# Performance work log

Hardware: AMD Instinct MI355X
Metric: run time of the kernel (lower is better)

The kernel has to match this reference:

```python
import jax, jax.numpy as jnp
import numpy as np

# ---- ATSSPostProcessor config ----
PRE_NMS_THRESH = 0.05
PRE_NMS_TOP_N  = 400      # k candidates per image (pre_nms_top_n)
NMS_THRESH     = 0.4
POST_TOP_N     = 100      # fpn_post_nms_top_n
MIN_SIZE       = 0.0
NUM_ANGLE_BINS = 90
BBOX_W         = (10.0, 10.0, 5.0, 5.0)   # box_coder xywh weights; angle is passthrough (argmax-90 deg)
N, C, H, W     = 4, 15, 256, 256           # A=1 anchor per location
STRIDE, ANCHOR_SIZE = 8.0, 64.0
MAXV = 16                                   # vertex buffer for quad-quad clipping


def setup_inputs():
    key = jax.random.key(0)
    k1, k2, k3, k4 = jax.random.split(key, 4)
    box_cls = jax.random.normal(k1, (N, C, H, W), jnp.float32) - 2.0  # sigmoid ~0.12 avg -> plenty of candidates
    box_regression = jax.random.normal(k2, (N, 4, H, W), jnp.float32) * 0.5
    centerness = jax.random.normal(k3, (N, 1, H, W), jnp.float32)
    angle = jax.random.normal(k4, (N, NUM_ANGLE_BINS, H, W), jnp.float32)
    # xywha anchors on the stride-8 grid, row-major (H, W) to match permute_and_flatten ordering
    ys, xs = jnp.meshgrid(jnp.arange(H, dtype=jnp.float32), jnp.arange(W, dtype=jnp.float32), indexing='ij')
    cx = (xs.reshape(-1) + 0.5) * STRIDE
    cy = (ys.reshape(-1) + 0.5) * STRIDE
    wh = jnp.full((H * W,), ANCHOR_SIZE, jnp.float32)
    a0 = jnp.zeros((H * W,), jnp.float32)
    anchors = jnp.broadcast_to(jnp.stack([cx, cy, wh, wh, a0], -1), (N, H * W, 5))
    return {"box_cls": box_cls, "box_regression": box_regression, "centerness": centerness,
            "angle": angle, "anchors": jnp.asarray(anchors)}


def xywha_to_corners(b):
    # b [..., 5] (cx,cy,w,h,angle_deg) -> [..., 4, 2], CCW order
    cx, cy, w, h, a = b[..., 0], b[..., 1], b[..., 2], b[..., 3], b[..., 4]
    t = a * (jnp.pi / 180.0)
    c, s = jnp.cos(t), jnp.sin(t)
    ox = jnp.asarray([1., -1., -1., 1.], b.dtype) * (w[..., None] * 0.5)
    oy = jnp.asarray([1., 1., -1., -1.], b.dtype) * (h[..., None] * 0.5)
    x = cx[..., None] + ox * c[..., None] - oy * s[..., None]
    y = cy[..., None] + ox * s[..., None] + oy * c[..., None]
    return jnp.stack([x, y], -1)


def _clip_edge(poly, n, p1, p2):
    # Sutherland-Hodgman: clip CCW polygon (poly[:n]) against half-plane left of p1->p2
    e = p2 - p1
    d = e[0] * (poly[:, 1] - p1[1]) - e[1] * (poly[:, 0] - p1[0])  # >= 0 is inside
    def body(i, carry):
        out, m = carry
        j = jnp.where(i == n - 1, 0, i + 1)
        cur, nxt, dc, dn = poly[i], poly[j], d[i], d[j]
        denom = dc - dn
        denom = jnp.where(jnp.abs(denom) < 1e-8, 1e-8, denom)
        ip = cur + (dc / denom) * (nxt - cur)
        act = i < n
        a1 = act & (dc >= 0)
        out = out.at[m].set(jnp.where(a1, cur, out[m]))
        m = m + a1.astype(jnp.int32)
        a2 = act & ((dc >= 0) != (dn >= 0))
        out = out.at[m].set(jnp.where(a2, ip, out[m]))
        m = m + a2.astype(jnp.int32)
        return out, m
    return jax.lax.fori_loop(0, 8, body, (jnp.zeros_like(poly), jnp.int32(0)))


def _quad_inter_area(c1, c2):
    # intersection area of two CCW quads via polygon clipping + shoelace
    poly = jnp.zeros((MAXV, 2), c1.dtype).at[:4].set(c1)
    n = jnp.int32(4)
    def edge(e, carry):
        poly, n = carry
        return _clip_edge(poly, n, c2[e], c2[(e + 1) % 4])
    poly, n = jax.lax.fori_loop(0, 4, edge, (poly, n))
    idx = jnp.arange(MAXV)
    j = jnp.where(idx == n - 1, 0, idx + 1)
    mask = idx < n
    terms = poly[:, 0] * poly[j, 1] - poly[j, 0] * poly[:, 1]
    return 0.5 * jnp.abs(jnp.sum(jnp.where(mask, terms, 0.0)))


def _riou_matrix(boxes):                        # [k,5] -> [k,k] rotated IoU
    corners = xywha_to_corners(boxes)           # [k,4,2]
    areas = boxes[:, 2] * boxes[:, 3]
    def one(ci, ai):
        def two(cj, aj):
            inter = _quad_inter_area(ci, cj)
            return inter / (ai + aj - inter + 1e-7)
        return jax.vmap(two)(corners, areas)
    return jax.vmap(one)(corners, areas)


@jax.jit
def _forward(box_cls, box_regression, centerness, angle, anchors):
    n, c, h, w = box_cls.shape
    K, k = h * w, PRE_NMS_TOP_N
    # permute_and_flatten + activations
    cls = jax.nn.sigmoid(box_cls).transpose(0, 2, 3, 1).reshape(n, K, c)
    reg = box_regression.transpose(0, 2, 3, 1).reshape(n, K, 4)
    ctr = jax.nn.sigmoid(centerness).reshape(n, K)
    ang = jax.nn.softmax(angle.transpose(0, 2, 3, 1).reshape(n, K, NUM_ANGLE_BINS), axis=-1)
    # pre-nms threshold on raw sigmoid cls, topk on cls*centerness
    cand = cls > PRE_NMS_THRESH
    comb = cls * ctr[:, :, None]
    flat = jnp.where(cand, comb, -1.0).reshape(n, K * c)
    topv, topi = jax.lax.top_k(flat, k)          # sorted descending
    valid = topv > 0.0                           # emulates per_pre_nms_top_n clamp
    loc = topi // c
    labels = topi % c + 1
    reg_s = jnp.take_along_axis(reg, loc[..., None], axis=1)       # [n,k,4]
    anc_s = jnp.take_along_axis(anchors, loc[..., None], axis=1)   # [n,k,5]
    ang_s = jnp.take_along_axis(ang, loc[..., None], axis=1)       # [n,k,90]
    pred_angle = jnp.argmax(ang_s, axis=-1).astype(reg_s.dtype) - 90.0
    # box_coder.decode (xywh deltas, angle passthrough)
    wx, wy, ww, wh = BBOX_W
    dx, dy = reg_s[..., 0] / wx, reg_s[..., 1] / wy
    dw = jnp.clip(reg_s[..., 2] / ww, -10.0, 4.0)
    dh = jnp.clip(reg_s[..., 3] / wh, -10.0, 4.0)
    acx, acy, aw, ah = anc_s[..., 0], anc_s[..., 1], anc_s[..., 2], anc_s[..., 3]
    boxes = jnp.stack([dx * aw + acx, dy * ah + acy,
                       aw * jnp.exp(dw), ah * jnp.exp(dh), pred_angle], -1)
    valid = valid & (boxes[..., 2] >= MIN_SIZE) & (boxes[..., 3] >= MIN_SIZE)
    scores = jnp.where(valid, jnp.sqrt(jnp.maximum(topv, 0.0)), 0.0)
    # class-aware rotated NMS (boxlist_ml_rnms): IoU only within same class
    iou = jax.lax.stop_gradient(jax.vmap(_riou_matrix)(boxes))     # [n,k,k]
    same = labels[:, :, None] == labels[:, None, :]
    iou = jnp.where(same, iou, 0.0)
    idxs = jnp.arange(k)
    def body(i, keep):
        sup = keep[:, i][:, None] & (iou[:, i, :] > NMS_THRESH) & (idxs[None, :] > i)
        return keep & ~sup
    keep = jax.lax.fori_loop(0, k, body, valid)
    # keep top fpn_post_nms_top_n by score
    fscore = jnp.where(keep, scores, -1.0)
    fv, fi = jax.lax.top_k(fscore, POST_TOP_N)
    fvalid = fv > 0.0
    fboxes = jnp.take_along_axis(boxes, fi[..., None], axis=1)
    flabels = jnp.take_along_axis(labels, fi, axis=1)
    corners = xywha_to_corners(fboxes).reshape(n, POST_TOP_N, 8)   # convert('xyxyxyxy')
    out = jnp.concatenate([corners,
                           jnp.maximum(fv, 0.0)[..., None],
                           flabels.astype(corners.dtype)[..., None],
                           fvalid.astype(corners.dtype)[..., None]], -1)
    return out * fvalid[..., None].astype(out.dtype)   # [N, POST_TOP_N, 11]


def reference(box_cls, box_regression, centerness, angle, anchors):
    return _forward(box_cls, box_regression, centerness, angle, anchors)
```

## Files before the change

### kernel.cpp

```cpp
#include <hip/hip_runtime.h>
#include <math.h>

#define NIMG 4
#define NCLS 15
#define HW 65536
#define NANG 90
#define KTOP 400
#define POSTN 100
#define NBINS 4096
#define CAP 4096

#define HIST_OFF   0
#define CNT_OFF    65536
#define SUPT_OFF   65600
#define ZERO_BYTES 165952
#define CAND_OFF   165952
#define SKEY_OFF   297024
#define COR_OFF    309824
#define AREA_OFF   361024
#define LAB_OFF    367424
#define SC_OFF     373824
#define VAL_OFF    380224
#define CCX_OFF    386624
#define CCY_OFF    393024
#define CRAD_OFF   399424

__device__ __forceinline__ float sigmoidf(float x) {
    return 1.0f / (1.0f + expf(-x));
}

__global__ __launch_bounds__(256)
void k_hist(const float* __restrict__ cls, const float* __restrict__ ctr,
            int* __restrict__ hist) {
    __shared__ int sh[NBINS];
    const int n = blockIdx.y;
    const int p2 = (blockIdx.x * 256 + threadIdx.x) * 2;
    for (int b = threadIdx.x; b < NBINS; b += 256) sh[b] = 0;
    __syncthreads();
    float2 cv2 = *(const float2*)(ctr + n * HW + p2);
    float cv[2] = {sigmoidf(cv2.x), sigmoidf(cv2.y)};
    for (int j = 0; j < NCLS; ++j) {
        float2 s2 = *(const float2*)(cls + (size_t)(n * NCLS + j) * HW + p2);
        float sv[2] = {s2.x, s2.y};
#pragma unroll
        for (int e = 0; e < 2; ++e) {
            float s = sigmoidf(sv[e]);
            if (s > 0.05f) {
                float comb = s * cv[e];
                int b = (int)(comb * 4096.0f);
                b = b < 0 ? 0 : (b > NBINS - 1 ? NBINS - 1 : b);
                atomicAdd(&sh[b], 1);
            }
        }
    }
    __syncthreads();
    for (int b = threadIdx.x; b < NBINS; b += 256) {
        int v = sh[b];
        if (v) atomicAdd(&hist[n * NBINS + b], v);
    }
}

__global__ __launch_bounds__(256)
void k_collect(const float* __restrict__ cls, const float* __restrict__ ctr,
               const int* __restrict__ hist, int* __restrict__ cnt,
               unsigned long long* __restrict__ cand) {
    const int n = blockIdx.y;
    __shared__ int part[256];
    __shared__ int s_t;
    {
        const int* hb = hist + n * NBINS;
        int s = 0;
        int base = threadIdx.x * 16;
        for (int b = 0; b < 16; ++b) s += hb[base + b];
        part[threadIdx.x] = s;
        if (threadIdx.x == 0) s_t = 0;
        __syncthreads();
        for (int off = 1; off < 256; off <<= 1) {
            int v = part[threadIdx.x] +
                    ((threadIdx.x + off < 256) ? part[threadIdx.x + off] : 0);
            __syncthreads();
            part[threadIdx.x] = v;
            __syncthreads();
        }
        int sg = threadIdx.x;
        int suf = part[sg];
        int above = (sg == 255) ? 0 : part[sg + 1];
        if (suf >= KTOP && above < KTOP) {
            int a2 = above, t = sg * 16;
            for (int b = sg * 16 + 15; b >= sg * 16; --b) {
                a2 += hb[b];
                if (a2 >= KTOP) { t = b; break; }
            }
            s_t = t;
        }
        __syncthreads();
    }
    const int t = s_t;
    const int p2 = (blockIdx.x * 256 + threadIdx.x) * 2;
    float2 cv2 = *(const float2*)(ctr + n * HW + p2);
    float cv[2] = {sigmoidf(cv2.x), sigmoidf(cv2.y)};
    for (int j = 0; j < NCLS; ++j) {
        float2 s2 = *(const float2*)(cls + (size_t)(n * NCLS + j) * HW + p2);
        float sv[2] = {s2.x, s2.y};
#pragma unroll
        for (int e = 0; e < 2; ++e) {
            float s = sigmoidf(sv[e]);
            if (s > 0.05f) {
                float comb = s * cv[e];
                int b = (int)(comb * 4096.0f);
                b = b < 0 ? 0 : (b > NBINS - 1 ? NBINS - 1 : b);
                if (b >= t) {
                    int pos = atomicAdd(&cnt[n], 1);
                    if (pos < CAP) {
                        unsigned int fb  = __float_as_uint(comb);
                        unsigned int idx = (unsigned int)((p2 + e) * NCLS + j);
                        cand[n * CAP + pos] =
                            ((unsigned long long)fb << 32) | (unsigned long long)(~idx);
                    }
                }
            }
        }
    }
}

__global__ __launch_bounds__(256)
void k_select(const unsigned long long* __restrict__ cand, const int* __restrict__ cnt,
              unsigned long long* __restrict__ skey) {
    const int n = blockIdx.x;
    __shared__ unsigned long long key[CAP];
    int c = cnt[n];
    if (c > CAP) c = CAP;
    int S = 512;
    while (S < c) S <<= 1;
    for (int t = threadIdx.x; t < S; t += 256)
        key[t] = (t < c) ? cand[n * CAP + t] : 0ULL;
    __syncthreads();
    for (int k = 2; k <= S; k <<= 1) {
        for (int j = k >> 1; j > 0; j >>= 1) {
            for (int i = threadIdx.x; i < S; i += 256) {
                int l = i ^ j;
                if (l > i) {
                    unsigned long long a = key[i], b = key[l];
                    bool up = ((i & k) == 0);
                    if ((a > b) == up) { key[i] = b; key[l] = a; }
                }
            }
            __syncthreads();
        }
    }
    for (int r = threadIdx.x; r < KTOP; r += 256)
        skey[n * KTOP + r] = key[S - 1 - r];
}

__global__ __launch_bounds__(64)
void k_decode(const unsigned long long* __restrict__ skey,
              const float* __restrict__ reg, const float* __restrict__ ang,
              const float* __restrict__ anchors,
              float* __restrict__ cor, float* __restrict__ area, int* __restrict__ lab,
              float* __restrict__ sc, int* __restrict__ val,
              float* __restrict__ ccx, float* __restrict__ ccy, float* __restrict__ crad) {
#pragma clang fp contract(off)
    const int r = blockIdx.x;
    const int n = blockIdx.y;
    const int l = threadIdx.x;
    const int base = n * KTOP + r;
    unsigned long long kk = skey[base];
    if (kk == 0ULL) {
        if (l == 0) {
            val[base] = 0; sc[base] = 0.0f; lab[base] = 0; area[base] = 0.0f;
            ccx[base] = 0.0f; ccy[base] = 0.0f; crad[base] = 0.0f;
            for (int q = 0; q < 8; ++q) cor[base * 8 + q] = 0.0f;
        }
        return;
    }
    unsigned int idx = ~((unsigned int)kk);
    int loc = (int)(idx / 15u);
    const float* ap = ang + ((size_t)n * NANG) * HW + loc;
    float bv = -INFINITY; int bb = 1000;
    for (int b = l; b < NANG; b += 64) {
        float v = ap[(size_t)b * HW];
        if (v > bv) { bv = v; bb = b; }
    }
    for (int off = 32; off > 0; off >>= 1) {
        float ov = __shfl_down(bv, off);
        int   ob = __shfl_down(bb, off);
        if (ov > bv || (ov == bv && ob < bb)) { bv = ov; bb = ob; }
    }
    if (l == 0) {
        int cl = (int)(idx % 15u);
        float topv = __uint_as_float((unsigned int)(kk >> 32));
        const float* rp = reg + ((size_t)n * 4) * HW + loc;
        float dx = rp[0] / 10.0f;
        float dy = rp[HW] / 10.0f;
        float dw = rp[2 * (size_t)HW] / 5.0f;
        float dh = rp[3 * (size_t)HW] / 5.0f;
        dw = fminf(fmaxf(dw, -10.0f), 4.0f);
        dh = fminf(fmaxf(dh, -10.0f), 4.0f);
        const float* an = anchors + ((size_t)n * HW + loc) * 5;
        float acx = an[0], acy = an[1], aw = an[2], ah = an[3];
        float bcx = dx * aw + acx;
        float bcy = dy * ah + acy;
        float bw = aw * expf(dw);
        float bh = ah * expf(dh);
        float pa = (float)bb - 90.0f;
        float th = pa * (float)0.017453292519943295;
        float cth = cosf(th), sth = sinf(th);
        float hw2 = bw * 0.5f, hh2 = bh * 0.5f;
        const float oxs[4] = {1.0f, -1.0f, -1.0f, 1.0f};
        const float oys[4] = {1.0f, 1.0f, -1.0f, -1.0f};
        for (int q = 0; q < 4; ++q) {
            float ox = oxs[q] * hw2, oy = oys[q] * hh2;
            cor[base * 8 + 2 * q]     = bcx + ox * cth - oy * sth;
            cor[base * 8 + 2 * q + 1] = bcy + ox * sth + oy * cth;
        }
        val[base] = 1;
        sc[base] = sqrtf(topv);
        lab[base] = cl + 1;
        area[base] = bw * bh;
        ccx[base] = bcx; ccy[base] = bcy;
        crad[base] = 0.5f * sqrtf(bw * bw + bh * bh);
    }
}

__device__ __forceinline__ float arr_get8(const float* a, int idx) {
    float r = a[0];
#pragma unroll
    for (int s = 1; s < 8; ++s) r = (s == idx) ? a[s] : r;
    return r;
}
__device__ __forceinline__ void arr_set8(float* a, int idx, float v) {
#pragma unroll
    for (int s = 0; s < 8; ++s) a[s] = (s == idx) ? v : a[s];
}

__device__ float quad_inter_area(const float* c1x, const float* c1y,
                                 const float* c2x, const float* c2y) {
#pragma clang fp contract(off)
    float px[8], py[8], qx[8], qy[8];
    int n = 4;
#pragma unroll
    for (int i = 0; i < 8; ++i) { px[i] = (i < 4) ? c1x[i] : 0.0f;
                                  py[i] = (i < 4) ? c1y[i] : 0.0f;
                                  qx[i] = 0.0f; qy[i] = 0.0f; }
#pragma unroll
    for (int e = 0; e < 4; ++e) {
        float p1x = c2x[e], p1y = c2y[e];
        int e2 = (e + 1) & 3;
        float ex = c2x[e2] - p1x, ey = c2y[e2] - p1y;
        int m = 0;
#pragma unroll
        for (int i = 0; i < 8; ++i) {
            if (i < n) {
                int j = (i == n - 1) ? 0 : i + 1;
                float cxi = px[i], cyi = py[i];
                float cxj = arr_get8(px, j), cyj = arr_get8(py, j);
                float dc = ex * (cyi - p1y) - ey * (cxi - p1x);
                float dn = ex * (cyj - p1y) - ey * (cxj - p1x);
                bool ic = (dc >= 0.0f), in2 = (dn >= 0.0f);
                if (ic) { arr_set8(qx, m, cxi); arr_set8(qy, m, cyi); ++m; }
                if (ic != in2) {
                    float denom = dc - dn;
                    if (fabsf(denom) < 1e-8f) denom = 1e-8f;
                    float tp = dc / denom;
                    arr_set8(qx, m, cxi + tp * (cxj - cxi));
                    arr_set8(qy, m, cyi + tp * (cyj - cyi));
                    ++m;
                }
            }
        }
        n = m;
        if (n == 0) return 0.0f;
#pragma unroll
        for (int i = 0; i < 8; ++i) { px[i] = qx[i]; py[i] = qy[i]; }
    }
    float ssum = 0.0f;
#pragma unroll
    for (int i = 0; i < 8; ++i) {
        if (i < n) {
            int j = (i == n - 1) ? 0 : i + 1;
            ssum += px[i] * arr_get8(py, j) - arr_get8(px, j) * py[i];
        }
    }
    return 0.5f * fabsf(ssum);
}

__global__ __launch_bounds__(256)
void k_pairs(const float* __restrict__ cor, const float* __restrict__ area,
             const int* __restrict__ lab,
             const float* __restrict__ ccx, const float* __restrict__ ccy,
             const float* __restrict__ crad,
             unsigned long long* __restrict__ supT) {
#pragma clang fp contract(off)
    const int n = blockIdx.y;
    const int p = blockIdx.x * 256 + threadIdx.x;
    if (p >= KTOP * KTOP) return;
    const int i = p / KTOP;
    const int j = p - i * KTOP;
    if (j <= i) return;
    const int base = n * KTOP;
    const int li = lab[base + i];
    if (li == 0 || lab[base + j] != li) return;
    float dx = ccx[base + i] - ccx[base + j];
    float dy = ccy[base + i] - ccy[base + j];
    float rr = crad[base + i] + crad[base + j];
    if (dx * dx + dy * dy > rr * rr) return;
    float cix[4], ciy[4], cjx[4], cjy[4];
    for (int q = 0; q < 4; ++q) {
        cix[q] = cor[(base + i) * 8 + 2 * q]; ciy[q] = cor[(base + i) * 8 + 2 * q + 1];
        cjx[q] = cor[(base + j) * 8 + 2 * q]; cjy[q] = cor[(base + j) * 8 + 2 * q + 1];
    }
    float inter = quad_inter_area(cix, ciy, cjx, cjy);
    float iou = inter / (area[base + i] + area[base + j] - inter + 1e-7f);
    if (iou > 0.4f) {
        atomicOr(&supT[((size_t)(n * 7 + (j >> 6)) * 7 + (i >> 6)) * 64 + (j & 63)],
                 1ULL << (i & 63));
    }
}

__global__ __launch_bounds__(64)
void k_nms_out(const unsigned long long* __restrict__ supT,
               const int* __restrict__ val,
               const float* __restrict__ cor, const float* __restrict__ sc,
               const int* __restrict__ lab, float* __restrict__ out) {
    const int n = blockIdx.x;
    const int l = threadIdx.x;
    unsigned removed = 0;
#pragma unroll
    for (int t = 0; t < 7; ++t) {
        int r = 64 * t + l;
        int v = (r < KTOP) ? val[n * KTOP + r] : 0;
        if (!v) removed |= (1u << t);
    }
    unsigned long long cm[7][7];
#pragma unroll
    for (int t = 0; t < 7; ++t)
#pragma unroll
        for (int rb = 0; rb < 7; ++rb)
            cm[t][rb] = supT[((size_t)(n * 7 + t) * 7 + rb) * 64 + l];
#pragma unroll
    for (int rb = 0; rb < 7; ++rb) {
        const int lim = (rb == 6) ? (KTOP - 384) : 64;
        for (int ib = 0; ib < lim; ++ib) {
            unsigned rm = (unsigned)__builtin_amdgcn_readlane((int)removed, ib);
            if (!((rm >> rb) & 1u)) {
                removed |= ((unsigned)((cm[0][rb] >> ib) & 1ULL));
                removed |= ((unsigned)((cm[1][rb] >> ib) & 1ULL)) << 1;
                removed |= ((unsigned)((cm[2][rb] >> ib) & 1ULL)) << 2;
                removed |= ((unsigned)((cm[3][rb] >> ib) & 1ULL)) << 3;
                removed |= ((unsigned)((cm[4][rb] >> ib) & 1ULL)) << 4;
                removed |= ((unsigned)((cm[5][rb] >> ib) & 1ULL)) << 5;
                removed |= ((unsigned)((cm[6][rb] >> ib) & 1ULL)) << 6;
            }
        }
    }
    __shared__ int order[POSTN];
    int rank = 0;
#pragma unroll
    for (int t = 0; t < 7; ++t) {
        bool kb = !((removed >> t) & 1u) && (64 * t + l < KTOP);
        unsigned long long m = __ballot(kb);
        int my = rank + __popcll(m & ((1ULL << l) - 1ULL));
        if (kb && my < POSTN) order[my] = 64 * t + l;
        rank += __popcll(m);
    }
    int kcnt = rank < POSTN ? rank : POSTN;
    __syncthreads();
    for (int e = l; e < POSTN * 11; e += 64) {
        int r = e / 11, c = e - r * 11;
        float v = 0.0f;
        if (r < kcnt) {
            int i = order[r];
            int b = n * KTOP + i;
            if (c < 8)       v = cor[b * 8 + c];
            else if (c == 8) v = sc[b];
            else if (c == 9) v = (float)lab[b];
            else             v = 1.0f;
        }
        out[(n * POSTN + r) * 11 + c] = v;
    }
}

extern "C" void kernel_launch(void* const* d_in, const int* in_sizes, int n_in,
                              void* d_out, int out_size, void* d_ws, size_t ws_size,
                              hipStream_t stream) {
    const float* box_cls = (const float*)d_in[0];
    const float* box_reg = (const float*)d_in[1];
    const float* ctr     = (const float*)d_in[2];
    const float* ang     = (const float*)d_in[3];
    const float* anchors = (const float*)d_in[4];
    float* out = (float*)d_out;
    char* ws = (char*)d_ws;

    int* hist = (int*)(ws + HIST_OFF);
    int* cnt  = (int*)(ws + CNT_OFF);
    unsigned long long* supT = (unsigned long long*)(ws + SUPT_OFF);
    unsigned long long* cand = (unsigned long long*)(ws + CAND_OFF);
    unsigned long long* skey = (unsigned long long*)(ws + SKEY_OFF);
    float* cor  = (float*)(ws + COR_OFF);
    float* area = (float*)(ws + AREA_OFF);
    int* lab    = (int*)(ws + LAB_OFF);
    float* sc   = (float*)(ws + SC_OFF);
    int* val    = (int*)(ws + VAL_OFF);
    float* ccx  = (float*)(ws + CCX_OFF);
    float* ccy  = (float*)(ws + CCY_OFF);
    float* crad = (float*)(ws + CRAD_OFF);

    hipMemsetAsync(d_ws, 0, ZERO_BYTES, stream);
    k_hist   <<<dim3(HW / 512, NIMG), 256, 0, stream>>>(box_cls, ctr, hist);
    k_collect<<<dim3(HW / 512, NIMG), 256, 0, stream>>>(box_cls, ctr, hist, cnt, cand);
    k_select <<<NIMG, 256, 0, stream>>>(cand, cnt, skey);
    k_decode <<<dim3(KTOP, NIMG), 64, 0, stream>>>(skey, box_reg, ang, anchors,
                                                   cor, area, lab, sc, val, ccx, ccy, crad);
    k_pairs  <<<dim3((KTOP * KTOP + 255) / 256, NIMG), 256, 0, stream>>>(
                 cor, area, lab, ccx, ccy, crad, supT);
    k_nms_out<<<NIMG, 64, 0, stream>>>(supT, val, cor, sc, lab, out);
}
```

Baseline: 248.8 us.

## Fuse histogram and collect into cooperative kernel; merge sort with decode

Replaces the memset, histogram and collect kernels with one cooperative kernel. It zeroes the workspace in-kernel, keeps the per-pixel combined scores in registers, and uses two grid-wide syncs instead of separate launches. The bitonic sort and box decode are merged into one kernel, so sorted keys go straight from shared memory to decode without a global skey buffer. The cost is that decode now runs on only 4 blocks with serial 90-bin angle argmax per thread instead of 1600 wave-parallel blocks, and the cooperative launch requires all 512 blocks to be co-resident. Blocks also add their partial histograms to hist after only one grid sync following the zeroing, which is correct but tightly ordered.

```diff
diff --git a/kernel.cpp b/kernel.cpp
--- a/kernel.cpp
+++ b/kernel.cpp
@@ -1,5 +1,8 @@
 #include <hip/hip_runtime.h>
+#include <hip/hip_cooperative_groups.h>
 #include <math.h>
+
+namespace cg = cooperative_groups;
 
 #define NIMG 4
 #define NCLS 15
@@ -15,7 +18,6 @@
 #define SUPT_OFF   65600
 #define ZERO_BYTES 165952
 #define CAND_OFF   165952
-#define SKEY_OFF   297024
 #define COR_OFF    309824
 #define AREA_OFF   361024
 #define LAB_OFF    367424
@@ -30,43 +32,56 @@
 }
 
 __global__ __launch_bounds__(256)
-void k_hist(const float* __restrict__ cls, const float* __restrict__ ctr,
-            int* __restrict__ hist) {
-    __shared__ int sh[NBINS];
+void k_fused_select(const float* __restrict__ cls, const float* __restrict__ ctr,
+                    int* wsz, int* hist, int* cnt,
+                    unsigned long long* __restrict__ cand) {
+    __shared__ int sh[2][NBINS];
+    __shared__ int part[256];
+    __shared__ int s_t;
     const int n = blockIdx.y;
     const int p2 = (blockIdx.x * 256 + threadIdx.x) * 2;
-    for (int b = threadIdx.x; b < NBINS; b += 256) sh[b] = 0;
+
+    {
+        const int gtid = (blockIdx.y * gridDim.x + blockIdx.x) * 256 + threadIdx.x;
+        for (int z = gtid; z < (ZERO_BYTES / 4); z += 131072) wsz[z] = 0;
+    }
+    for (int b = threadIdx.x; b < NBINS; b += 256) { sh[0][b] = 0; sh[1][b] = 0; }
+
+    float cb[15][2];
+    {
+        float2 cv2 = *(const float2*)(ctr + n * HW + p2);
+        float cv0 = sigmoidf(cv2.x), cv1 = sigmoidf(cv2.y);
+#pragma unroll
+        for (int j = 0; j < NCLS; ++j) {
+            float2 s2 = *(const float2*)(cls + (size_t)(n * NCLS + j) * HW + p2);
+            float s0 = sigmoidf(s2.x), s1 = sigmoidf(s2.y);
+            cb[j][0] = (s0 > 0.05f) ? s0 * cv0 : -1.0f;
+            cb[j][1] = (s1 > 0.05f) ? s1 * cv1 : -1.0f;
+        }
+    }
     __syncthreads();
-    float2 cv2 = *(const float2*)(ctr + n * HW + p2);
-    float cv[2] = {sigmoidf(cv2.x), sigmoidf(cv2.y)};
+    const int subh = threadIdx.x & 1;
+#pragma unroll
     for (int j = 0; j < NCLS; ++j) {
-        float2 s2 = *(const float2*)(cls + (size_t)(n * NCLS + j) * HW + p2);
-        float sv[2] = {s2.x, s2.y};
 #pragma unroll
         for (int e = 0; e < 2; ++e) {
-            float s = sigmoidf(sv[e]);
-            if (s > 0.05f) {
-                float comb = s * cv[e];
-                int b = (int)(comb * 4096.0f);
+            float c = cb[j][e];
+            if (c >= 0.0f) {
+                int b = (int)(c * 4096.0f);
                 b = b < 0 ? 0 : (b > NBINS - 1 ? NBINS - 1 : b);
-                atomicAdd(&sh[b], 1);
+                atomicAdd(&sh[subh][b], 1);
             }
         }
     }
     __syncthreads();
+    cg::this_grid().sync();
+
     for (int b = threadIdx.x; b < NBINS; b += 256) {
-        int v = sh[b];
+        int v = sh[0][b] + sh[1][b];
         if (v) atomicAdd(&hist[n * NBINS + b], v);
     }
-}
-
-__global__ __launch_bounds__(256)
-void k_collect(const float* __restrict__ cls, const float* __restrict__ ctr,
-               const int* __restrict__ hist, int* __restrict__ cnt,
-               unsigned long long* __restrict__ cand) {
-    const int n = blockIdx.y;
-    __shared__ int part[256];
-    __shared__ int s_t;
+    cg::this_grid().sync();
+
     {
         const int* hb = hist + n * NBINS;
         int s = 0;
@@ -96,23 +111,18 @@
         __syncthreads();
     }
     const int t = s_t;
-    const int p2 = (blockIdx.x * 256 + threadIdx.x) * 2;
-    float2 cv2 = *(const float2*)(ctr + n * HW + p2);
-    float cv[2] = {sigmoidf(cv2.x), sigmoidf(cv2.y)};
+#pragma unroll
     for (int j = 0; j < NCLS; ++j) {
-        float2 s2 = *(const float2*)(cls + (size_t)(n * NCLS + j) * HW + p2);
-        float sv[2] = {s2.x, s2.y};
 #pragma unroll
         for (int e = 0; e < 2; ++e) {
-            float s = sigmoidf(sv[e]);
-            if (s > 0.05f) {
-                float comb = s * cv[e];
-                int b = (int)(comb * 4096.0f);
+            float c = cb[j][e];
+            if (c >= 0.0f) {
+                int b = (int)(c * 4096.0f);
                 b = b < 0 ? 0 : (b > NBINS - 1 ? NBINS - 1 : b);
                 if (b >= t) {
                     int pos = atomicAdd(&cnt[n], 1);
                     if (pos < CAP) {
-                        unsigned int fb  = __float_as_uint(comb);
+                        unsigned int fb  = __float_as_uint(c);
                         unsigned int idx = (unsigned int)((p2 + e) * NCLS + j);
                         cand[n * CAP + pos] =
                             ((unsigned long long)fb << 32) | (unsigned long long)(~idx);
@@ -124,8 +134,13 @@
 }
 
 __global__ __launch_bounds__(256)
-void k_select(const unsigned long long* __restrict__ cand, const int* __restrict__ cnt,
-              unsigned long long* __restrict__ skey) {
+void k_sortdecode(const unsigned long long* __restrict__ cand, const int* __restrict__ cnt,
+                  const float* __restrict__ reg, const float* __restrict__ ang,
+                  const float* __restrict__ anchors,
+                  float* __restrict__ cor, float* __restrict__ area, int* __restrict__ lab,
+                  float* __restrict__ sc, int* __restrict__ val,
+                  float* __restrict__ ccx, float* __restrict__ ccy, float* __restrict__ crad) {
+#pragma clang fp contract(off)
     const int n = blockIdx.x;
     __shared__ unsigned long long key[CAP];
     int c = cnt[n];
@@ -148,45 +163,24 @@
             __syncthreads();
         }
     }
-    for (int r = threadIdx.x; r < KTOP; r += 256)
-        skey[n * KTOP + r] = key[S - 1 - r];
-}
-
-__global__ __launch_bounds__(64)
-void k_decode(const unsigned long long* __restrict__ skey,
-              const float* __restrict__ reg, const float* __restrict__ ang,
-              const float* __restrict__ anchors,
-              float* __restrict__ cor, float* __restrict__ area, int* __restrict__ lab,
-              float* __restrict__ sc, int* __restrict__ val,
-              float* __restrict__ ccx, float* __restrict__ ccy, float* __restrict__ crad) {
-#pragma clang fp contract(off)
-    const int r = blockIdx.x;
-    const int n = blockIdx.y;
-    const int l = threadIdx.x;
-    const int base = n * KTOP + r;
-    unsigned long long kk = skey[base];
-    if (kk == 0ULL) {
-        if (l == 0) {
+    for (int r = threadIdx.x; r < KTOP; r += 256) {
+        const int base = n * KTOP + r;
+        unsigned long long kk = key[S - 1 - r];
+        if (kk == 0ULL) {
             val[base] = 0; sc[base] = 0.0f; lab[base] = 0; area[base] = 0.0f;
             ccx[base] = 0.0f; ccy[base] = 0.0f; crad[base] = 0.0f;
             for (int q = 0; q < 8; ++q) cor[base * 8 + q] = 0.0f;
-        }
-        return;
-    }
-    unsigned int idx = ~((unsigned int)kk);
-    int loc = (int)(idx / 15u);
-    const float* ap = ang + ((size_t)n * NANG) * HW + loc;
-    float bv = -INFINITY; int bb = 1000;
-    for (int b = l; b < NANG; b += 64) {
-        float v = ap[(size_t)b * HW];
-        if (v > bv) { bv = v; bb = b; }
-    }
-    for (int off = 32; off > 0; off >>= 1) {
-        float ov = __shfl_down(bv, off);
-        int   ob = __shfl_down(bb, off);
-        if (ov > bv || (ov == bv && ob < bb)) { bv = ov; bb = ob; }
-    }
-    if (l == 0) {
+            continue;
+        }
+        unsigned int idx = ~((unsigned int)kk);
+        int loc = (int)(idx / 15u);
+        const float* ap = ang + ((size_t)n * NANG) * HW + loc;
+        float bv = -INFINITY; int bb = 0;
+#pragma unroll
+        for (int b = 0; b < NANG; ++b) {
+            float v = ap[(size_t)b * HW];
+            if (v > bv) { bv = v; bb = b; }
+        }
         int cl = (int)(idx % 15u);
         float topv = __uint_as_float((unsigned int)(kk >> 32));
         const float* rp = reg + ((size_t)n * 4) * HW + loc;
@@ -208,6 +202,7 @@
         float hw2 = bw * 0.5f, hh2 = bh * 0.5f;
         const float oxs[4] = {1.0f, -1.0f, -1.0f, 1.0f};
         const float oys[4] = {1.0f, 1.0f, -1.0f, -1.0f};
+#pragma unroll
         for (int q = 0; q < 4; ++q) {
             float ox = oxs[q] * hw2, oy = oys[q] * hh2;
             cor[base * 8 + 2 * q]     = bcx + ox * cth - oy * sth;
@@ -391,11 +386,11 @@
     float* out = (float*)d_out;
     char* ws = (char*)d_ws;
 
+    int* wsz  = (int*)(ws + HIST_OFF);
     int* hist = (int*)(ws + HIST_OFF);
     int* cnt  = (int*)(ws + CNT_OFF);
     unsigned long long* supT = (unsigned long long*)(ws + SUPT_OFF);
     unsigned long long* cand = (unsigned long long*)(ws + CAND_OFF);
-    unsigned long long* skey = (unsigned long long*)(ws + SKEY_OFF);
     float* cor  = (float*)(ws + COR_OFF);
     float* area = (float*)(ws + AREA_OFF);
     int* lab    = (int*)(ws + LAB_OFF);
@@ -405,13 +400,15 @@
     float* ccy  = (float*)(ws + CCY_OFF);
     float* crad = (float*)(ws + CRAD_OFF);
 
-    hipMemsetAsync(d_ws, 0, ZERO_BYTES, stream);
-    k_hist   <<<dim3(HW / 512, NIMG), 256, 0, stream>>>(box_cls, ctr, hist);
-    k_collect<<<dim3(HW / 512, NIMG), 256, 0, stream>>>(box_cls, ctr, hist, cnt, cand);
-    k_select <<<NIMG, 256, 0, stream>>>(cand, cnt, skey);
-    k_decode <<<dim3(KTOP, NIMG), 64, 0, stream>>>(skey, box_reg, ang, anchors,
-                                                   cor, area, lab, sc, val, ccx, ccy, crad);
-    k_pairs  <<<dim3((KTOP * KTOP + 255) / 256, NIMG), 256, 0, stream>>>(
-                 cor, area, lab, ccx, ccy, crad, supT);
+    {
+        void* args[] = {(void*)&box_cls, (void*)&ctr, (void*)&wsz,
+                        (void*)&hist, (void*)&cnt, (void*)&cand};
+        hipLaunchCooperativeKernel((const void*)k_fused_select,
+                                   dim3(HW / 512, NIMG), dim3(256), args, 0, stream);
+    }
+    k_sortdecode<<<NIMG, 256, 0, stream>>>(cand, cnt, box_reg, ang, anchors,
+                                           cor, area, lab, sc, val, ccx, ccy, crad);
+    k_pairs<<<dim3((KTOP * KTOP + 255) / 256, NIMG), 256, 0, stream>>>(
+             cor, area, lab, ccx, ccy, crad, supT);
     k_nms_out<<<NIMG, 64, 0, stream>>>(supT, val, cor, sc, lab, out);
 }
```

After: 470.3 us. 89.0% more time.

## Stage high-score candidates during histogram pass and merge collect into select

Applied to the files above, without the earlier changes.

The histogram kernel now also writes candidates above a fixed score-bin floor into a per-image staging buffer. This removes the second full pass over the class and centerness tensors that the collect kernel used to make. A new combined select kernel filters the staged entries by the top-k threshold and sorts them in shared memory. It falls back to a single-block full rescan when the staging overflows or the threshold falls below the floor. The supT zeroing also moves from the memset into the decode kernel to shrink the memset, and one kernel launch is removed. The fixed floor bin is tuned to the expected score distribution, so if it is wrong the slow single-block fallback runs.

```diff
diff --git a/kernel.cpp b/kernel.cpp
--- a/kernel.cpp
+++ b/kernel.cpp
@@ -9,21 +9,25 @@
 #define POSTN 100
 #define NBINS 4096
 #define CAP 4096
+#define SCAP 49152
+#define SBUF 512
+#define FLOOR_BIN 1434
 
 #define HIST_OFF   0
-#define CNT_OFF    65536
+#define SCNT_OFF   65536
+#define SFLAG_OFF  65552
+#define ZERO_BYTES 65600
 #define SUPT_OFF   65600
-#define ZERO_BYTES 165952
-#define CAND_OFF   165952
-#define SKEY_OFF   297024
-#define COR_OFF    309824
-#define AREA_OFF   361024
-#define LAB_OFF    367424
-#define SC_OFF     373824
-#define VAL_OFF    380224
-#define CCX_OFF    386624
-#define CCY_OFF    393024
-#define CRAD_OFF   399424
+#define STAGE_OFF  165952
+#define SKEY_OFF   1738816
+#define COR_OFF    1751616
+#define AREA_OFF   1802816
+#define LAB_OFF    1809216
+#define SC_OFF     1815616
+#define VAL_OFF    1822016
+#define CCX_OFF    1828416
+#define CCY_OFF    1834816
+#define CRAD_OFF   1841216
 
 __device__ __forceinline__ float sigmoidf(float x) {
     return 1.0f / (1.0f + expf(-x));
@@ -31,11 +35,15 @@
 
 __global__ __launch_bounds__(256)
 void k_hist(const float* __restrict__ cls, const float* __restrict__ ctr,
-            int* __restrict__ hist) {
+            int* __restrict__ hist, int* __restrict__ scnt,
+            unsigned long long* __restrict__ stage, int* __restrict__ sflag) {
     __shared__ int sh[NBINS];
+    __shared__ unsigned long long sbuf[SBUF];
+    __shared__ int scount, sbase;
     const int n = blockIdx.y;
     const int p2 = (blockIdx.x * 256 + threadIdx.x) * 2;
     for (int b = threadIdx.x; b < NBINS; b += 256) sh[b] = 0;
+    if (threadIdx.x == 0) scount = 0;
     __syncthreads();
     float2 cv2 = *(const float2*)(ctr + n * HW + p2);
     float cv[2] = {sigmoidf(cv2.x), sigmoidf(cv2.y)};
@@ -50,6 +58,15 @@
                 int b = (int)(comb * 4096.0f);
                 b = b < 0 ? 0 : (b > NBINS - 1 ? NBINS - 1 : b);
                 atomicAdd(&sh[b], 1);
+                if (b >= FLOOR_BIN) {
+                    int m = atomicAdd(&scount, 1);
+                    if (m < SBUF) {
+                        unsigned int fb  = __float_as_uint(comb);
+                        unsigned int idx = (unsigned int)((p2 + e) * NCLS + j);
+                        sbuf[m] = ((unsigned long long)fb << 32) |
+                                  (unsigned long long)(~idx);
+                    }
+                }
             }
         }
     }
@@ -58,22 +75,36 @@
         int v = sh[b];
         if (v) atomicAdd(&hist[n * NBINS + b], v);
     }
+    if (threadIdx.x == 0) {
+        int c = scount;
+        if (c > SBUF) { atomicOr(sflag, 1); c = SBUF; }
+        sbase = atomicAdd(&scnt[n], c);
+    }
+    __syncthreads();
+    int c = scount < SBUF ? scount : SBUF;
+    int base = sbase;
+    for (int m = threadIdx.x; m < c; m += 256) {
+        int g = base + m;
+        if (g < SCAP) stage[n * SCAP + g] = sbuf[m];
+    }
 }
 
 __global__ __launch_bounds__(256)
-void k_collect(const float* __restrict__ cls, const float* __restrict__ ctr,
-               const int* __restrict__ hist, int* __restrict__ cnt,
-               unsigned long long* __restrict__ cand) {
-    const int n = blockIdx.y;
+void k_selstage(const unsigned long long* __restrict__ stage, const int* __restrict__ scnt,
+                const int* __restrict__ sflag, const int* __restrict__ hist,
+                const float* __restrict__ cls, const float* __restrict__ ctr,
+                unsigned long long* __restrict__ skey) {
+    const int n = blockIdx.x;
+    __shared__ unsigned long long key[CAP];
     __shared__ int part[256];
-    __shared__ int s_t;
+    __shared__ int s_t, s_c;
+    const int* hb = hist + n * NBINS;
     {
-        const int* hb = hist + n * NBINS;
         int s = 0;
         int base = threadIdx.x * 16;
         for (int b = 0; b < 16; ++b) s += hb[base + b];
         part[threadIdx.x] = s;
-        if (threadIdx.x == 0) s_t = 0;
+        if (threadIdx.x == 0) { s_t = 0; s_c = 0; }
         __syncthreads();
         for (int off = 1; off < 256; off <<= 1) {
             int v = part[threadIdx.x] +
@@ -96,44 +127,47 @@
         __syncthreads();
     }
     const int t = s_t;
-    const int p2 = (blockIdx.x * 256 + threadIdx.x) * 2;
-    float2 cv2 = *(const float2*)(ctr + n * HW + p2);
-    float cv[2] = {sigmoidf(cv2.x), sigmoidf(cv2.y)};
-    for (int j = 0; j < NCLS; ++j) {
-        float2 s2 = *(const float2*)(cls + (size_t)(n * NCLS + j) * HW + p2);
-        float sv[2] = {s2.x, s2.y};
-#pragma unroll
-        for (int e = 0; e < 2; ++e) {
-            float s = sigmoidf(sv[e]);
-            if (s > 0.05f) {
-                float comb = s * cv[e];
-                int b = (int)(comb * 4096.0f);
-                b = b < 0 ? 0 : (b > NBINS - 1 ? NBINS - 1 : b);
-                if (b >= t) {
-                    int pos = atomicAdd(&cnt[n], 1);
-                    if (pos < CAP) {
-                        unsigned int fb  = __float_as_uint(comb);
-                        unsigned int idx = (unsigned int)((p2 + e) * NCLS + j);
-                        cand[n * CAP + pos] =
-                            ((unsigned long long)fb << 32) | (unsigned long long)(~idx);
+    const bool fb = (sflag[0] != 0) || (scnt[n] > SCAP) || (t < FLOOR_BIN);
+    if (!fb) {
+        const int sc = scnt[n];
+        for (int m = threadIdx.x; m < sc; m += 256) {
+            unsigned long long kk = stage[n * SCAP + m];
+            float comb = __uint_as_float((unsigned int)(kk >> 32));
+            int b = (int)(comb * 4096.0f);
+            b = b < 0 ? 0 : (b > NBINS - 1 ? NBINS - 1 : b);
+            if (b >= t) {
+                int pos = atomicAdd(&s_c, 1);
+                if (pos < CAP) key[pos] = kk;
+            }
+        }
+    } else {
+        for (int j = 0; j < NCLS; ++j) {
+            for (int pos = threadIdx.x; pos < HW; pos += 256) {
+                float s = sigmoidf(cls[(size_t)(n * NCLS + j) * HW + pos]);
+                if (s > 0.05f) {
+                    float comb = s * sigmoidf(ctr[n * HW + pos]);
+                    int b = (int)(comb * 4096.0f);
+                    b = b < 0 ? 0 : (b > NBINS - 1 ? NBINS - 1 : b);
+                    if (b >= t) {
+                        int p = atomicAdd(&s_c, 1);
+                        if (p < CAP) {
+                            unsigned int fbits = __float_as_uint(comb);
+                            unsigned int idx = (unsigned int)(pos * NCLS + j);
+                            key[p] = ((unsigned long long)fbits << 32) |
+                                     (unsigned long long)(~idx);
+                        }
                     }
                 }
             }
         }
     }
-}
-
-__global__ __launch_bounds__(256)
-void k_select(const unsigned long long* __restrict__ cand, const int* __restrict__ cnt,
-              unsigned long long* __restrict__ skey) {
-    const int n = blockIdx.x;
-    __shared__ unsigned long long key[CAP];
-    int c = cnt[n];
+    __syncthreads();
+    int c = s_c;
     if (c > CAP) c = CAP;
     int S = 512;
     while (S < c) S <<= 1;
-    for (int t = threadIdx.x; t < S; t += 256)
-        key[t] = (t < c) ? cand[n * CAP + t] : 0ULL;
+    for (int i = threadIdx.x; i < S; i += 256)
+        if (i >= c) key[i] = 0ULL;
     __syncthreads();
     for (int k = 2; k <= S; k <<= 1) {
         for (int j = k >> 1; j > 0; j >>= 1) {
@@ -158,11 +192,17 @@
               const float* __restrict__ anchors,
               float* __restrict__ cor, float* __restrict__ area, int* __restrict__ lab,
               float* __restrict__ sc, int* __restrict__ val,
-              float* __restrict__ ccx, float* __restrict__ ccy, float* __restrict__ crad) {
+              float* __restrict__ ccx, float* __restrict__ ccy, float* __restrict__ crad,
+              unsigned long long* __restrict__ supT) {
 #pragma clang fp contract(off)
     const int r = blockIdx.x;
     const int n = blockIdx.y;
     const int l = threadIdx.x;
+    {
+        int bid = n * KTOP + r;
+        int z = bid * 8 + l;
+        if (l < 8 && z < 12544) supT[z] = 0ULL;
+    }
     const int base = n * KTOP + r;
     unsigned long long kk = skey[base];
     if (kk == 0ULL) {
@@ -391,11 +431,12 @@
     float* out = (float*)d_out;
     char* ws = (char*)d_ws;
 
-    int* hist = (int*)(ws + HIST_OFF);
-    int* cnt  = (int*)(ws + CNT_OFF);
-    unsigned long long* supT = (unsigned long long*)(ws + SUPT_OFF);
-    unsigned long long* cand = (unsigned long long*)(ws + CAND_OFF);
-    unsigned long long* skey = (unsigned long long*)(ws + SKEY_OFF);
+    int* hist  = (int*)(ws + HIST_OFF);
+    int* scnt  = (int*)(ws + SCNT_OFF);
+    int* sflag = (int*)(ws + SFLAG_OFF);
+    unsigned long long* supT  = (unsigned long long*)(ws + SUPT_OFF);
+    unsigned long long* stage = (unsigned long long*)(ws + STAGE_OFF);
+    unsigned long long* skey  = (unsigned long long*)(ws + SKEY_OFF);
     float* cor  = (float*)(ws + COR_OFF);
     float* area = (float*)(ws + AREA_OFF);
     int* lab    = (int*)(ws + LAB_OFF);
@@ -406,12 +447,14 @@
     float* crad = (float*)(ws + CRAD_OFF);
 
     hipMemsetAsync(d_ws, 0, ZERO_BYTES, stream);
-    k_hist   <<<dim3(HW / 512, NIMG), 256, 0, stream>>>(box_cls, ctr, hist);
-    k_collect<<<dim3(HW / 512, NIMG), 256, 0, stream>>>(box_cls, ctr, hist, cnt, cand);
-    k_select <<<NIMG, 256, 0, stream>>>(cand, cnt, skey);
-    k_decode <<<dim3(KTOP, NIMG), 64, 0, stream>>>(skey, box_reg, ang, anchors,
-                                                   cor, area, lab, sc, val, ccx, ccy, crad);
-    k_pairs  <<<dim3((KTOP * KTOP + 255) / 256, NIMG), 256, 0, stream>>>(
-                 cor, area, lab, ccx, ccy, crad, supT);
-    k_nms_out<<<NIMG, 64, 0, stream>>>(supT, val, cor, sc, lab, out);
-}
+    k_hist    <<<dim3(HW / 512, NIMG), 256, 0, stream>>>(box_cls, ctr, hist,
+                                                         scnt, stage, sflag);
+    k_selstage<<<NIMG, 256, 0, stream>>>(stage, scnt, sflag, hist,
+                                         box_cls, ctr, skey);
+    k_decode  <<<dim3(KTOP, NIMG), 64, 0, stream>>>(skey, box_reg, ang, anchors,
+                                                    cor, area, lab, sc, val,
+                                                    ccx, ccy, crad, supT);
+    k_pairs   <<<dim3((KTOP * KTOP + 255) / 256, NIMG), 256, 0, stream>>>(
+                  cor, area, lab, ccx, ccy, crad, supT);
+    k_nms_out <<<NIMG, 64, 0, stream>>>(supT, val, cor, sc, lab, out);
+}
```

New measurement: 248.4 us. No clear change (-0.2%).
